# Kernel optimization log

Measured on AMD Instinct MI355X. Metric: run time of the kernel, lower is better.

## Reference

```python
import jax, jax.numpy as jnp
import numpy as np

N_DIM = 32
N_HEADS = 4
HEAD_SIZE = N_DIM // N_HEADS  # 8


def setup_inputs() -> dict:
    key = jax.random.key(0)
    ks = jax.random.split(key, 9)
    B, T = 16, 2048
    s = 1.0 / np.sqrt(N_DIM)
    inp = {
        "x": jax.random.normal(ks[0], (B, T, N_DIM), dtype=jnp.float32),
        "Wq": jax.random.uniform(ks[1], (N_DIM, N_DIM), jnp.float32, -s, s),
        "bq": jax.random.uniform(ks[2], (N_DIM,), jnp.float32, -s, s),
        "Wk": jax.random.uniform(ks[3], (N_DIM, N_DIM), jnp.float32, -s, s),
        "bk": jax.random.uniform(ks[4], (N_DIM,), jnp.float32, -s, s),
        "Wv": jax.random.uniform(ks[5], (N_DIM, N_DIM), jnp.float32, -s, s),
        "bv": jax.random.uniform(ks[6], (N_DIM,), jnp.float32, -s, s),
        "Wp": jax.random.uniform(ks[7], (N_DIM, N_DIM), jnp.float32, -s, s),
        "bp": jax.random.uniform(ks[8], (N_DIM,), jnp.float32, -s, s),
    }
    return inp


def reference(x, Wq, bq, Wk, bk, Wv, bv, Wp, bp):
    b, t, c = x.shape
    # nn.Linear: y = x @ W^T + b
    def heads(W, bias):
        y = jnp.einsum("btc,dc->btd", x, W) + bias
        return y.reshape(b, t, N_HEADS, HEAD_SIZE).transpose(0, 2, 1, 3)  # [b,h,t,d]

    q = heads(Wq, bq)
    k = heads(Wk, bk)
    v = heads(Wv, bv)

    scores = jnp.einsum("bhqd,bhkd->bhqk", q, k) / np.sqrt(HEAD_SIZE)  # [b,h,t,t]
    causal = jnp.tril(jnp.ones((t, t), dtype=bool))
    scores = jnp.where(causal[None, None], scores, -jnp.inf)
    weights = jax.nn.softmax(scores, axis=-1)
    # dropout layers are identity in eval mode
    z = jnp.einsum("bhqk,bhkd->bhqd", weights, v)
    z = z.transpose(0, 2, 1, 3).reshape(b, t, N_DIM)
    z = jnp.einsum("btc,dc->btd", z, Wp) + bp
    return z
```

## Files before the change

### kernel.cpp

```cpp
#include <hip/hip_runtime.h>
#include <math.h>

#define BB 16
#define TT 2048
#define CC 32
#define HH 4
#define DD 8

#define KBS 2056
#define VRS 264
#define VBS (9 * VRS)
#define ZP 33

typedef __fp16 h2  __attribute__((ext_vector_type(2)));
typedef __fp16 h8  __attribute__((ext_vector_type(8)));
typedef float  fx16 __attribute__((ext_vector_type(16)));
typedef int    i4v __attribute__((ext_vector_type(4)));

__device__ __forceinline__ h2 pkh(float a, float b) {
#if __has_builtin(__builtin_amdgcn_cvt_pkrtz)
    return __builtin_amdgcn_cvt_pkrtz(a, b);
#else
    h2 r; r.x = (__fp16)a; r.y = (__fp16)b; return r;
#endif
}

__device__ __forceinline__ float fexp2(float x) {
#if __has_builtin(__builtin_amdgcn_exp2f)
    return __builtin_amdgcn_exp2f(x);
#else
    return exp2f(x);
#endif
}

__device__ __forceinline__ int h2bits(h2 v) { return __builtin_bit_cast(int, v); }

__device__ __forceinline__ void makeP(const fx16& S, bool last, int thr, int hi, h8* P) {
    float pe[16];
    #pragma unroll
    for (int r = 0; r < 16; r++) {
        const int ko = (r & 3) + 8 * (r >> 2);
        float sv = S[r];
        if (last) sv = (ko <= thr) ? sv : -INFINITY;
        pe[r] = fexp2(sv);
    }
    int Hh[8];
    #pragma unroll
    for (int i = 0; i < 8; i++) Hh[i] = h2bits(pkh(pe[2*i], pe[2*i+1]));
    #pragma unroll
    for (int s = 0; s < 2; s++) {
        const int b0 = 4 * s;
        int own0 = hi ? Hh[b0+2] : Hh[b0+0];
        int own1 = hi ? Hh[b0+3] : Hh[b0+1];
        int snd0 = hi ? Hh[b0+0] : Hh[b0+2];
        int snd1 = hi ? Hh[b0+1] : Hh[b0+3];
        int rcv0 = __shfl_xor(snd0, 32);
        int rcv1 = __shfl_xor(snd1, 32);
        i4v f;
        f.x = hi ? rcv0 : own0;
        f.y = hi ? rcv1 : own1;
        f.z = hi ? own0 : rcv0;
        f.w = hi ? own1 : rcv1;
        P[s] = __builtin_bit_cast(h8, f);
    }
}

__global__ __launch_bounds__(256) void qkv_kernel(
    const float* __restrict__ x,
    const float* __restrict__ Wq, const float* __restrict__ bq,
    const float* __restrict__ Wk, const float* __restrict__ bk,
    const float* __restrict__ Wv, const float* __restrict__ bv,
    __fp16* __restrict__ Qo, __fp16* __restrict__ Ko, __fp16* __restrict__ Vo)
{
    __shared__ float Xs[256 * ZP];
    const int tid = threadIdx.x;
    const int m = blockIdx.y >> 2, h = blockIdx.y & 3;
    const int row0 = blockIdx.x * 256;

    {
        const float4* xg = (const float4*)(x + (size_t)row0 * CC);
        #pragma unroll
        for (int i = 0; i < 8; i++) {
            const int idx = tid + 256 * i;
            float4 f = xg[idx];
            const int w = idx * 4;
            float* d = &Xs[(w >> 5) * ZP + (w & 31)];
            d[0] = f.x; d[1] = f.y; d[2] = f.z; d[3] = f.w;
        }
    }
    __syncthreads();

    const int row = row0 + tid;
    const int b = row >> 11, t = row & 2047;
    const int bh = b * HH + h;

    float xr[CC];
    #pragma unroll
    for (int c = 0; c < CC; c++) xr[c] = Xs[tid * ZP + c];

    const float* W    = (m == 0) ? Wq : (m == 1) ? Wk : Wv;
    const float* bias = (m == 0) ? bq : (m == 1) ? bk : bv;

    float o[DD];
    #pragma unroll
    for (int d = 0; d < DD; d++) {
        const int dd = h * DD + d;
        float acc = bias[dd];
        #pragma unroll
        for (int c = 0; c < CC; c++) acc += xr[c] * W[dd * CC + c];
        o[d] = acc;
    }

    if (m == 0) {
        const float qs = 0.3535533905932738f * 1.4426950408889634f;
        i4v qw;
        qw.x = h2bits(pkh(o[0]*qs, o[1]*qs)); qw.y = h2bits(pkh(o[2]*qs, o[3]*qs));
        qw.z = h2bits(pkh(o[4]*qs, o[5]*qs)); qw.w = h2bits(pkh(o[6]*qs, o[7]*qs));
        *(i4v*)(Qo + ((size_t)bh * TT + t) * DD) = qw;
    } else if (m == 1) {
        i4v kw;
        kw.x = h2bits(pkh(o[0], o[1])); kw.y = h2bits(pkh(o[2], o[3]));
        kw.z = h2bits(pkh(o[4], o[5])); kw.w = h2bits(pkh(o[6], o[7]));
        *(i4v*)(Ko + ((size_t)bh * TT + t) * DD) = kw;
    } else {
        __fp16* vt = Vo + (size_t)bh * 9 * TT + t;
        #pragma unroll
        for (int d = 0; d < DD; d++) vt[d * TT] = (__fp16)o[d];
        vt[8 * TT] = (__fp16)1.0f;
    }
}

__global__ __launch_bounds__(256, 2) void attn_kernel(
    const __fp16* __restrict__ Qg, const __fp16* __restrict__ Kg,
    const __fp16* __restrict__ Vg,
    const float* __restrict__ Wp, const float* __restrict__ bp,
    float* __restrict__ out)
{
    __shared__ __align__(16) __fp16 KsS[4 * KBS];
    __shared__ __align__(16) __fp16 VtS[4 * VBS];
    __shared__ float zbuf[64 * ZP];

    const int tid  = threadIdx.x;
    const int b    = blockIdx.x & 15;
    const int ip   = blockIdx.x >> 4;
    const int h    = tid >> 6;
    const int lane = tid & 63;
    const int qc   = lane & 31;
    const int hi   = lane >> 5;

    const int bh  = b * HH + h;
    const int qb1 = 32 * ip;
    const int qb2 = 32 * (63 - ip);
    const int keys_needed = qb2 + 32;
    const int nst = (keys_needed + 255) >> 8;

    h8 qf1, qf2;
    {
        h8 qz;
        #pragma unroll
        for (int i = 0; i < 8; i++) qz[i] = (__fp16)0.0f;
        h8 qa = *(const h8*)(Qg + ((size_t)bh * TT + qb1 + qc) * DD);
        h8 qb = *(const h8*)(Qg + ((size_t)bh * TT + qb2 + qc) * DD);
        qf1 = hi ? qz : qa;
        qf2 = hi ? qz : qb;
    }

    fx16 O1, O2, zc;
    #pragma unroll
    for (int i = 0; i < 16; i++) { O1[i] = 0.0f; O2[i] = 0.0f; zc[i] = 0.0f; }

    const int vrow = (qc < 9) ? qc : 8;
    const int thr  = qc - 4 * hi;

    const __fp16* kgl = Kg + (size_t)bh * TT * DD;
    const __fp16* vgl = Vg + (size_t)bh * 9 * TT;
    __fp16* kld = KsS + h * KBS;
    __fp16* vld = VtS + h * VBS;
    const __fp16* kb = kld + qc * DD;
    const __fp16* vb = vld + vrow * VRS + 8 * hi;

    i4v kpre[4], vpre[5];
    {
        const i4v* ks = (const i4v*)kgl;
        #pragma unroll
        for (int r = 0; r < 4; r++) kpre[r] = ks[lane + 64 * r];
        #pragma unroll
        for (int r = 0; r < 5; r++) {
            int i = lane + 64 * r; if (i > 287) i = 287;
            vpre[r] = *(const i4v*)(vgl + (i >> 5) * TT + (i & 31) * 8);
        }
    }

    for (int sti = 0; sti < nst; sti++) {
        const int st = sti * 256;
        {
            i4v* kd = (i4v*)kld;
            #pragma unroll
            for (int r = 0; r < 4; r++) kd[lane + 64 * r] = kpre[r];
            #pragma unroll
            for (int r = 0; r < 5; r++) {
                const int i = lane + 64 * r;
                if (i < 288) *(i4v*)(vld + (i >> 5) * VRS + (i & 31) * 8) = vpre[r];
            }
        }
        if (sti + 1 < nst) {
            const int st2 = st + 256;
            const i4v* ks = (const i4v*)(kgl + (size_t)st2 * DD);
            #pragma unroll
            for (int r = 0; r < 4; r++) kpre[r] = ks[lane + 64 * r];
            #pragma unroll
            for (int r = 0; r < 5; r++) {
                int i = lane + 64 * r; if (i > 287) i = 287;
                vpre[r] = *(const i4v*)(vgl + (i >> 5) * TT + st2 + (i & 31) * 8);
            }
        }

        const int kend = min(st + 256, keys_needed);
        for (int kt = st; kt < kend; kt += 32) {
            const bool a1 = (kt <= qb1);
            h8 kf = *(const h8*)(kb + (kt - st) * DD);

            h8 P1[2], P2[2];
            if (a1) {
                fx16 S = __builtin_amdgcn_mfma_f32_32x32x16_f16(kf, qf1, zc, 0, 0, 0);
                makeP(S, kt == qb1, thr, hi, P1);
            }
            {
                fx16 S = __builtin_amdgcn_mfma_f32_32x32x16_f16(kf, qf2, zc, 0, 0, 0);
                makeP(S, kt == qb2, thr, hi, P2);
            }
            #pragma unroll
            for (int s = 0; s < 2; s++) {
                h8 vf = *(const h8*)(vb + (kt - st) + 16 * s);
                if (a1) O1 = __builtin_amdgcn_mfma_f32_32x32x16_f16(vf, P1[s], O1, 0, 0, 0);
                O2 = __builtin_amdgcn_mfma_f32_32x32x16_f16(vf, P2[s], O2, 0, 0, 0);
            }
        }
    }

    {
        const float i1 = 1.0f / O1[4], i2 = 1.0f / O2[4];
        float* z1 = &zbuf[qc * ZP + h * DD + 4 * hi];
        float* z2 = &zbuf[(32 + qc) * ZP + h * DD + 4 * hi];
        z1[0] = O1[0]*i1; z1[1] = O1[1]*i1; z1[2] = O1[2]*i1; z1[3] = O1[3]*i1;
        z2[0] = O2[0]*i2; z2[1] = O2[1]*i2; z2[2] = O2[2]*i2; z2[3] = O2[3]*i2;
    }
    __syncthreads();

    {
        const int seg = tid >> 6;
        const int r = tid & 63;
        float zr[CC];
        #pragma unroll
        for (int c = 0; c < CC; c++) zr[c] = zbuf[r * ZP + c];
        float o[DD];
        #pragma unroll
        for (int d = 0; d < DD; d++) {
            const int dd = seg * DD + d;
            float acc = bp[dd];
            #pragma unroll
            for (int c = 0; c < CC; c++) acc += zr[c] * Wp[dd * CC + c];
            o[d] = acc;
        }
        const int qglob = (r < 32) ? (ip * 32 + r) : ((63 - ip) * 32 + (r - 32));
        float* dst = out + ((size_t)b * TT + qglob) * CC + seg * DD;
        ((float4*)dst)[0] = make_float4(o[0], o[1], o[2], o[3]);
        ((float4*)dst)[1] = make_float4(o[4], o[5], o[6], o[7]);
    }
}

extern "C" void kernel_launch(void* const* d_in, const int* in_sizes, int n_in,
                              void* d_out, int out_size, void* d_ws, size_t ws_size,
                              hipStream_t stream) {
    const float* x  = (const float*)d_in[0];
    const float* Wq = (const float*)d_in[1];
    const float* bq = (const float*)d_in[2];
    const float* Wk = (const float*)d_in[3];
    const float* bk = (const float*)d_in[4];
    const float* Wv = (const float*)d_in[5];
    const float* bv = (const float*)d_in[6];
    const float* Wp = (const float*)d_in[7];
    const float* bp = (const float*)d_in[8];
    float* out = (float*)d_out;

    const size_t NE = (size_t)BB * HH * TT * DD;
    __fp16* Qh = (__fp16*)d_ws;
    __fp16* Kh = Qh + NE;
    __fp16* Vt = Kh + NE;

    qkv_kernel<<<dim3(BB * TT / 256, 12), 256, 0, stream>>>(x, Wq, bq, Wk, bk, Wv, bv, Qh, Kh, Vt);
    attn_kernel<<<dim3(BB * 32), 256, 0, stream>>>(Qh, Kh, Vt, Wp, bp, out);
}
```

Before: 111.9 us.

## Split paired query tiles across separate waves with 512-thread attention blocks

Each attention block now runs 8 waves instead of 4. Each wave handles one head and one of the two paired query tiles (early or late), where before one wave handled both tiles in sequence. This raises wave-level parallelism and shortens the per-wave critical path. In exchange, K/V tiles are staged into LDS twice (once per wave pair), LDS use doubles, and waves within a block become imbalanced because the early-tile wave finishes sooner. The output projection is split across 8 segments of 4 columns each.

Result: slower. 127.3 us (+13.7%).

```diff
diff --git a/kernel.cpp b/kernel.cpp
--- a/kernel.cpp
+++ b/kernel.cpp
@@ -130,52 +130,51 @@
     }
 }
 
-__global__ __launch_bounds__(256, 2) void attn_kernel(
+__global__ __launch_bounds__(512, 4) void attn_kernel(
     const __fp16* __restrict__ Qg, const __fp16* __restrict__ Kg,
     const __fp16* __restrict__ Vg,
     const float* __restrict__ Wp, const float* __restrict__ bp,
     float* __restrict__ out)
 {
-    __shared__ __align__(16) __fp16 KsS[4 * KBS];
-    __shared__ __align__(16) __fp16 VtS[4 * VBS];
+    __shared__ __align__(16) __fp16 KsS[8 * KBS];
+    __shared__ __align__(16) __fp16 VtS[8 * VBS];
     __shared__ float zbuf[64 * ZP];
 
     const int tid  = threadIdx.x;
     const int b    = blockIdx.x & 15;
     const int ip   = blockIdx.x >> 4;
-    const int h    = tid >> 6;
+    const int w    = tid >> 6;
+    const int h    = w & 3;
+    const int qsel = w >> 2;
     const int lane = tid & 63;
     const int qc   = lane & 31;
     const int hi   = lane >> 5;
 
     const int bh  = b * HH + h;
-    const int qb1 = 32 * ip;
-    const int qb2 = 32 * (63 - ip);
-    const int keys_needed = qb2 + 32;
+    const int qb  = 32 * (qsel ? (63 - ip) : ip);
+    const int keys_needed = qb + 32;
     const int nst = (keys_needed + 255) >> 8;
 
-    h8 qf1, qf2;
+    h8 qf;
     {
         h8 qz;
         #pragma unroll
         for (int i = 0; i < 8; i++) qz[i] = (__fp16)0.0f;
-        h8 qa = *(const h8*)(Qg + ((size_t)bh * TT + qb1 + qc) * DD);
-        h8 qb = *(const h8*)(Qg + ((size_t)bh * TT + qb2 + qc) * DD);
-        qf1 = hi ? qz : qa;
-        qf2 = hi ? qz : qb;
-    }
-
-    fx16 O1, O2, zc;
-    #pragma unroll
-    for (int i = 0; i < 16; i++) { O1[i] = 0.0f; O2[i] = 0.0f; zc[i] = 0.0f; }
+        h8 qa = *(const h8*)(Qg + ((size_t)bh * TT + qb + qc) * DD);
+        qf = hi ? qz : qa;
+    }
+
+    fx16 O, zc;
+    #pragma unroll
+    for (int i = 0; i < 16; i++) { O[i] = 0.0f; zc[i] = 0.0f; }
 
     const int vrow = (qc < 9) ? qc : 8;
     const int thr  = qc - 4 * hi;
 
     const __fp16* kgl = Kg + (size_t)bh * TT * DD;
     const __fp16* vgl = Vg + (size_t)bh * 9 * TT;
-    __fp16* kld = KsS + h * KBS;
-    __fp16* vld = VtS + h * VBS;
+    __fp16* kld = KsS + w * KBS;
+    __fp16* vld = VtS + w * VBS;
     const __fp16* kb = kld + qc * DD;
     const __fp16* vb = vld + vrow * VRS + 8 * hi;
 
@@ -217,33 +216,22 @@
 
         const int kend = min(st + 256, keys_needed);
         for (int kt = st; kt < kend; kt += 32) {
-            const bool a1 = (kt <= qb1);
             h8 kf = *(const h8*)(kb + (kt - st) * DD);
-
-            h8 P1[2], P2[2];
-            if (a1) {
-                fx16 S = __builtin_amdgcn_mfma_f32_32x32x16_f16(kf, qf1, zc, 0, 0, 0);
-                makeP(S, kt == qb1, thr, hi, P1);
-            }
-            {
-                fx16 S = __builtin_amdgcn_mfma_f32_32x32x16_f16(kf, qf2, zc, 0, 0, 0);
-                makeP(S, kt == qb2, thr, hi, P2);
-            }
+            fx16 S = __builtin_amdgcn_mfma_f32_32x32x16_f16(kf, qf, zc, 0, 0, 0);
+            h8 P[2];
+            makeP(S, kt == qb, thr, hi, P);
             #pragma unroll
             for (int s = 0; s < 2; s++) {
                 h8 vf = *(const h8*)(vb + (kt - st) + 16 * s);
-                if (a1) O1 = __builtin_amdgcn_mfma_f32_32x32x16_f16(vf, P1[s], O1, 0, 0, 0);
-                O2 = __builtin_amdgcn_mfma_f32_32x32x16_f16(vf, P2[s], O2, 0, 0, 0);
+                O = __builtin_amdgcn_mfma_f32_32x32x16_f16(vf, P[s], O, 0, 0, 0);
             }
         }
     }
 
     {
-        const float i1 = 1.0f / O1[4], i2 = 1.0f / O2[4];
-        float* z1 = &zbuf[qc * ZP + h * DD + 4 * hi];
-        float* z2 = &zbuf[(32 + qc) * ZP + h * DD + 4 * hi];
-        z1[0] = O1[0]*i1; z1[1] = O1[1]*i1; z1[2] = O1[2]*i1; z1[3] = O1[3]*i1;
-        z2[0] = O2[0]*i2; z2[1] = O2[1]*i2; z2[2] = O2[2]*i2; z2[3] = O2[3]*i2;
+        const float inv = 1.0f / O[4];
+        float* z = &zbuf[(qsel * 32 + qc) * ZP + h * DD + 4 * hi];
+        z[0] = O[0]*inv; z[1] = O[1]*inv; z[2] = O[2]*inv; z[3] = O[3]*inv;
     }
     __syncthreads();
 
@@ -253,19 +241,18 @@
         float zr[CC];
         #pragma unroll
         for (int c = 0; c < CC; c++) zr[c] = zbuf[r * ZP + c];
-        float o[DD];
-        #pragma unroll
-        for (int d = 0; d < DD; d++) {
-            const int dd = seg * DD + d;
+        float o[4];
+        #pragma unroll
+        for (int d = 0; d < 4; d++) {
+            const int dd = seg * 4 + d;
             float acc = bp[dd];
             #pragma unroll
             for (int c = 0; c < CC; c++) acc += zr[c] * Wp[dd * CC + c];
             o[d] = acc;
         }
         const int qglob = (r < 32) ? (ip * 32 + r) : ((63 - ip) * 32 + (r - 32));
-        float* dst = out + ((size_t)b * TT + qglob) * CC + seg * DD;
-        ((float4*)dst)[0] = make_float4(o[0], o[1], o[2], o[3]);
-        ((float4*)dst)[1] = make_float4(o[4], o[5], o[6], o[7]);
+        float* dst = out + ((size_t)b * TT + qglob) * CC + seg * 4;
+        *(float4*)dst = make_float4(o[0], o[1], o[2], o[3]);
     }
 }
 
@@ -289,5 +276,5 @@
     __fp16* Vt = Kh + NE;
 
     qkv_kernel<<<dim3(BB * TT / 256, 12), 256, 0, stream>>>(x, Wq, bq, Wk, bk, Wv, bv, Qh, Kh, Vt);
-    attn_kernel<<<dim3(BB * 32), 256, 0, stream>>>(Qh, Kh, Vt, Wp, bp, out);
-}
+    attn_kernel<<<dim3(BB * 32), 512, 0, stream>>>(Qh, Kh, Vt, Wp, bp, out);
+}
```

## Compute QKV projection with fp16 MFMA and use permlane32 swap in softmax

Applied to the files above, without the earlier changes.

The QKV projection kernel is rewritten so each wave computes a 32-row by 32-output tile with two 32x32x16 fp16 MFMAs, replacing the scalar FMA loops over shared-memory-staged x. Each block of three waves handles Q, K and V for 32 rows, with fragments rearranged across half-waves before packed stores. The attention kernel's P-fragment construction uses permlane32_swap instead of two shuffles plus selects when the builtin is available. Inputs and weights are now rounded to fp16 before the projection, which lowers precision, and the V path writes with scattered 2-byte stores.

Result: faster. 106.0 us (-5.3%).

```diff
diff --git a/kernel.cpp b/kernel.cpp
--- a/kernel.cpp
+++ b/kernel.cpp
@@ -16,6 +16,7 @@
 typedef __fp16 h8  __attribute__((ext_vector_type(8)));
 typedef float  fx16 __attribute__((ext_vector_type(16)));
 typedef int    i4v __attribute__((ext_vector_type(4)));
+typedef int    i2v __attribute__((ext_vector_type(2)));
 
 __device__ __forceinline__ h2 pkh(float a, float b) {
 #if __has_builtin(__builtin_amdgcn_cvt_pkrtz)
@@ -35,6 +36,13 @@
 
 __device__ __forceinline__ int h2bits(h2 v) { return __builtin_bit_cast(int, v); }
 
+__device__ __forceinline__ h8 pk8(float4 a, float4 b) {
+    i4v f;
+    f.x = h2bits(pkh(a.x, a.y)); f.y = h2bits(pkh(a.z, a.w));
+    f.z = h2bits(pkh(b.x, b.y)); f.w = h2bits(pkh(b.z, b.w));
+    return __builtin_bit_cast(h8, f);
+}
+
 __device__ __forceinline__ void makeP(const fx16& S, bool last, int thr, int hi, h8* P) {
     float pe[16];
     #pragma unroll
@@ -47,6 +55,19 @@
     int Hh[8];
     #pragma unroll
     for (int i = 0; i < 8; i++) Hh[i] = h2bits(pkh(pe[2*i], pe[2*i+1]));
+#if __has_builtin(__builtin_amdgcn_permlane32_swap)
+    #pragma unroll
+    for (int s = 0; s < 2; s++) {
+        const int b0 = 4 * s;
+        auto ra = __builtin_amdgcn_permlane32_swap(Hh[b0+0], Hh[b0+2], false, false);
+        auto rb = __builtin_amdgcn_permlane32_swap(Hh[b0+1], Hh[b0+3], false, false);
+        i2v pa = __builtin_bit_cast(i2v, ra);
+        i2v pb = __builtin_bit_cast(i2v, rb);
+        i4v f;
+        f.x = pa.x; f.y = pb.x; f.z = pa.y; f.w = pb.y;
+        P[s] = __builtin_bit_cast(h8, f);
+    }
+#else
     #pragma unroll
     for (int s = 0; s < 2; s++) {
         const int b0 = 4 * s;
@@ -63,70 +84,109 @@
         f.w = hi ? own1 : rcv1;
         P[s] = __builtin_bit_cast(h8, f);
     }
-}
-
-__global__ __launch_bounds__(256) void qkv_kernel(
+#endif
+}
+
+__global__ __launch_bounds__(192, 3) void qkv_kernel(
     const float* __restrict__ x,
     const float* __restrict__ Wq, const float* __restrict__ bq,
     const float* __restrict__ Wk, const float* __restrict__ bk,
     const float* __restrict__ Wv, const float* __restrict__ bv,
     __fp16* __restrict__ Qo, __fp16* __restrict__ Ko, __fp16* __restrict__ Vo)
 {
-    __shared__ float Xs[256 * ZP];
-    const int tid = threadIdx.x;
-    const int m = blockIdx.y >> 2, h = blockIdx.y & 3;
-    const int row0 = blockIdx.x * 256;
-
-    {
-        const float4* xg = (const float4*)(x + (size_t)row0 * CC);
-        #pragma unroll
-        for (int i = 0; i < 8; i++) {
-            const int idx = tid + 256 * i;
-            float4 f = xg[idx];
-            const int w = idx * 4;
-            float* d = &Xs[(w >> 5) * ZP + (w & 31)];
-            d[0] = f.x; d[1] = f.y; d[2] = f.z; d[3] = f.w;
-        }
-    }
-    __syncthreads();
-
-    const int row = row0 + tid;
-    const int b = row >> 11, t = row & 2047;
-    const int bh = b * HH + h;
-
-    float xr[CC];
-    #pragma unroll
-    for (int c = 0; c < CC; c++) xr[c] = Xs[tid * ZP + c];
+    const int tid  = threadIdx.x;
+    const int m    = tid >> 6;
+    const int lane = tid & 63;
+    const int qc   = lane & 31;
+    const int hi   = lane >> 5;
+
+    const int row = blockIdx.x * 32 + qc;
+    const int b   = row >> 11, t = row & 2047;
 
     const float* W    = (m == 0) ? Wq : (m == 1) ? Wk : Wv;
     const float* bias = (m == 0) ? bq : (m == 1) ? bk : bv;
 
-    float o[DD];
-    #pragma unroll
-    for (int d = 0; d < DD; d++) {
-        const int dd = h * DD + d;
-        float acc = bias[dd];
-        #pragma unroll
-        for (int c = 0; c < CC; c++) acc += xr[c] * W[dd * CC + c];
-        o[d] = acc;
-    }
-
+    const float* xr = x + (size_t)row * CC + 8 * hi;
+    h8 B0 = pk8(*(const float4*)(xr),      *(const float4*)(xr + 4));
+    h8 B1 = pk8(*(const float4*)(xr + 16), *(const float4*)(xr + 20));
+
+    const float* wr = W + (size_t)qc * CC + 8 * hi;
+    h8 A0 = pk8(*(const float4*)(wr),      *(const float4*)(wr + 4));
+    h8 A1 = pk8(*(const float4*)(wr + 16), *(const float4*)(wr + 20));
+
+    fx16 zc;
+    #pragma unroll
+    for (int i = 0; i < 16; i++) zc[i] = 0.0f;
+    fx16 D = __builtin_amdgcn_mfma_f32_32x32x16_f16(A0, B0, zc, 0, 0, 0);
+    D = __builtin_amdgcn_mfma_f32_32x32x16_f16(A1, B1, D, 0, 0, 0);
+
+    float o[16];
+    {
+        float4 bb0 = *(const float4*)(bias + 0  + 4 * hi);
+        float4 bb1 = *(const float4*)(bias + 8  + 4 * hi);
+        float4 bb2 = *(const float4*)(bias + 16 + 4 * hi);
+        float4 bb3 = *(const float4*)(bias + 24 + 4 * hi);
+        const float* bbp[1];
+        o[0] = D[0] + bb0.x; o[1] = D[1] + bb0.y; o[2]  = D[2]  + bb0.z; o[3]  = D[3]  + bb0.w;
+        o[4] = D[4] + bb1.x; o[5] = D[5] + bb1.y; o[6]  = D[6]  + bb1.z; o[7]  = D[7]  + bb1.w;
+        o[8] = D[8] + bb2.x; o[9] = D[9] + bb2.y; o[10] = D[10] + bb2.z; o[11] = D[11] + bb2.w;
+        o[12] = D[12] + bb3.x; o[13] = D[13] + bb3.y; o[14] = D[14] + bb3.z; o[15] = D[15] + bb3.w;
+        (void)bbp;
+    }
     if (m == 0) {
         const float qs = 0.3535533905932738f * 1.4426950408889634f;
-        i4v qw;
-        qw.x = h2bits(pkh(o[0]*qs, o[1]*qs)); qw.y = h2bits(pkh(o[2]*qs, o[3]*qs));
-        qw.z = h2bits(pkh(o[4]*qs, o[5]*qs)); qw.w = h2bits(pkh(o[6]*qs, o[7]*qs));
-        *(i4v*)(Qo + ((size_t)bh * TT + t) * DD) = qw;
-    } else if (m == 1) {
-        i4v kw;
-        kw.x = h2bits(pkh(o[0], o[1])); kw.y = h2bits(pkh(o[2], o[3]));
-        kw.z = h2bits(pkh(o[4], o[5])); kw.w = h2bits(pkh(o[6], o[7]));
-        *(i4v*)(Ko + ((size_t)bh * TT + t) * DD) = kw;
+        #pragma unroll
+        for (int r = 0; r < 16; r++) o[r] *= qs;
+    }
+
+    if (m == 2) {
+        #pragma unroll
+        for (int r = 0; r < 16; r++) {
+            const int h = r >> 2, d = (r & 3) + 4 * hi;
+            Vo[(((size_t)(b * HH + h)) * 9 + d) * TT + t] = (__fp16)o[r];
+        }
+        const int hA = hi ? 2 : 0, hB = hi ? 3 : 1;
+        Vo[(((size_t)(b * HH + hA)) * 9 + 8) * TT + t] = (__fp16)1.0f;
+        Vo[(((size_t)(b * HH + hB)) * 9 + 8) * TT + t] = (__fp16)1.0f;
     } else {
-        __fp16* vt = Vo + (size_t)bh * 9 * TT + t;
-        #pragma unroll
-        for (int d = 0; d < DD; d++) vt[d * TT] = (__fp16)o[d];
-        vt[8 * TT] = (__fp16)1.0f;
+        int I0[4], I1[4];
+        #pragma unroll
+        for (int g = 0; g < 4; g++) {
+            I0[g] = h2bits(pkh(o[4*g + 0], o[4*g + 1]));
+            I1[g] = h2bits(pkh(o[4*g + 2], o[4*g + 3]));
+        }
+        i4v fr0, fr1, fr2, fr3;
+#if __has_builtin(__builtin_amdgcn_permlane32_swap)
+    #define MAKE_FRAG(g, out) { \
+        auto ra = __builtin_amdgcn_permlane32_swap(I0[g], I1[g], false, false); \
+        auto rb = __builtin_amdgcn_permlane32_swap(I1[g], I0[g], false, false); \
+        i2v p1 = __builtin_bit_cast(i2v, ra); \
+        i2v p2 = __builtin_bit_cast(i2v, rb); \
+        i4v f; \
+        f.x = hi ? p2.x : p1.x;   \
+        f.y = hi ? p1.x : p2.x;   \
+        f.z = hi ? p2.y : p1.y;   \
+        f.w = hi ? p1.y : p2.y;   \
+        out = f; }
+#else
+    #define MAKE_FRAG(g, out) { \
+        int s0 = __shfl_xor(I0[g], 32); \
+        int s1 = __shfl_xor(I1[g], 32); \
+        i4v f; \
+        f.x = hi ? s0 : I0[g]; \
+        f.y = hi ? s1 : I1[g]; \
+        f.z = hi ? I0[g] : s0; \
+        f.w = hi ? I1[g] : s1; \
+        out = f; }
+#endif
+        MAKE_FRAG(0, fr0); MAKE_FRAG(1, fr1); MAKE_FRAG(2, fr2); MAKE_FRAG(3, fr3);
+    #undef MAKE_FRAG
+        i4v fA = hi ? fr2 : fr0;
+        i4v fB = hi ? fr3 : fr1;
+        const int gA = hi ? 2 : 0, gB = hi ? 3 : 1;
+        __fp16* O = (m == 0) ? Qo : Ko;
+        *(i4v*)(O + ((size_t)(b * HH + gA) * TT + t) * DD) = fA;
+        *(i4v*)(O + ((size_t)(b * HH + gB) * TT + t) * DD) = fB;
     }
 }
 
@@ -288,6 +348,6 @@
     __fp16* Kh = Qh + NE;
     __fp16* Vt = Kh + NE;
 
-    qkv_kernel<<<dim3(BB * TT / 256, 12), 256, 0, stream>>>(x, Wq, bq, Wk, bk, Wv, bv, Qh, Kh, Vt);
+    qkv_kernel<<<dim3(BB * TT / 32), 192, 0, stream>>>(x, Wq, bq, Wk, bk, Wv, bv, Qh, Kh, Vt);
     attn_kernel<<<dim3(BB * 32), 256, 0, stream>>>(Qh, Kh, Vt, Wp, bp, out);
 }
```

## Fuse QKV projection into attention kernel, recomputing K/V per key tile via MFMA

Applied to the files above, without the earlier changes.

Removes the separate QKV kernel and its fp16 workspace round trip. Each attention block now projects Q, K and V on the fly from x using MFMA with fp16-packed weights. V is written into a small double-buffered LDS slot per key tile, and the next tile of x is prefetched. The cross-half-wave exchange uses permlane32_swap where the builtin is available. In exchange, every block redundantly recomputes K and V for all keys it needs, and LDS writes and reads of V happen within a wave without an explicit barrier.

Result: slower. 130.3 us (+16.5%).

```diff
diff --git a/kernel.cpp b/kernel.cpp
--- a/kernel.cpp
+++ b/kernel.cpp
@@ -7,15 +7,15 @@
 #define HH 4
 #define DD 8
 
-#define KBS 2056
-#define VRS 264
-#define VBS (9 * VRS)
+#define VR2 88
+#define VBS2 (9 * VR2)
 #define ZP 33
 
 typedef __fp16 h2  __attribute__((ext_vector_type(2)));
 typedef __fp16 h8  __attribute__((ext_vector_type(8)));
 typedef float  fx16 __attribute__((ext_vector_type(16)));
 typedef int    i4v __attribute__((ext_vector_type(4)));
+typedef int    i2v __attribute__((ext_vector_type(2)));
 
 __device__ __forceinline__ h2 pkh(float a, float b) {
 #if __has_builtin(__builtin_amdgcn_cvt_pkrtz)
@@ -34,6 +34,31 @@
 }
 
 __device__ __forceinline__ int h2bits(h2 v) { return __builtin_bit_cast(int, v); }
+
+__device__ __forceinline__ h8 pk8(float4 a, float4 b) {
+    i4v f;
+    f.x = h2bits(pkh(a.x, a.y)); f.y = h2bits(pkh(a.z, a.w));
+    f.z = h2bits(pkh(b.x, b.y)); f.w = h2bits(pkh(b.z, b.w));
+    return __builtin_bit_cast(h8, f);
+}
+
+__device__ __forceinline__ h8 rowfrag(float o0, float o1, float o2, float o3, int hi) {
+    int I0 = h2bits(pkh(o0, o1));
+    int I1 = h2bits(pkh(o2, o3));
+    i4v f;
+#if __has_builtin(__builtin_amdgcn_permlane32_swap)
+    auto ra = __builtin_amdgcn_permlane32_swap(I0, I0, false, false);
+    auto rb = __builtin_amdgcn_permlane32_swap(I1, I1, false, false);
+    i2v pa = __builtin_bit_cast(i2v, ra);
+    i2v pb = __builtin_bit_cast(i2v, rb);
+    f.x = I0; f.y = I1; f.z = pa.y; f.w = pb.y;
+#else
+    int s0 = __shfl_xor(I0, 32), s1 = __shfl_xor(I1, 32);
+    f.x = hi ? s0 : I0; f.y = hi ? s1 : I1;
+    f.z = hi ? I0 : s0; f.w = hi ? I1 : s1;
+#endif
+    return __builtin_bit_cast(h8, f);
+}
 
 __device__ __forceinline__ void makeP(const fx16& S, bool last, int thr, int hi, h8* P) {
     float pe[16];
@@ -47,6 +72,19 @@
     int Hh[8];
     #pragma unroll
     for (int i = 0; i < 8; i++) Hh[i] = h2bits(pkh(pe[2*i], pe[2*i+1]));
+#if __has_builtin(__builtin_amdgcn_permlane32_swap)
+    #pragma unroll
+    for (int s = 0; s < 2; s++) {
+        const int b0 = 4 * s;
+        auto ra = __builtin_amdgcn_permlane32_swap(Hh[b0+0], Hh[b0+2], false, false);
+        auto rb = __builtin_amdgcn_permlane32_swap(Hh[b0+1], Hh[b0+3], false, false);
+        i2v pa = __builtin_bit_cast(i2v, ra);
+        i2v pb = __builtin_bit_cast(i2v, rb);
+        i4v f;
+        f.x = pa.x; f.y = pb.x; f.z = pa.y; f.w = pb.y;
+        P[s] = __builtin_bit_cast(h8, f);
+    }
+#else
     #pragma unroll
     for (int s = 0; s < 2; s++) {
         const int b0 = 4 * s;
@@ -63,81 +101,28 @@
         f.w = hi ? own1 : rcv1;
         P[s] = __builtin_bit_cast(h8, f);
     }
-}
-
-__global__ __launch_bounds__(256) void qkv_kernel(
+#endif
+}
+
+struct XP { float4 a, b, c, d; };
+__device__ __forceinline__ XP load_xpack(const float* __restrict__ x,
+                                         int bTT, int t, int hi) {
+    const float* xr = x + (size_t)(bTT + t) * CC + 8 * hi;
+    XP p;
+    p.a = *(const float4*)(xr);      p.b = *(const float4*)(xr + 4);
+    p.c = *(const float4*)(xr + 16); p.d = *(const float4*)(xr + 20);
+    return p;
+}
+
+__global__ __launch_bounds__(256, 2) void attn_kernel(
     const float* __restrict__ x,
     const float* __restrict__ Wq, const float* __restrict__ bq,
     const float* __restrict__ Wk, const float* __restrict__ bk,
     const float* __restrict__ Wv, const float* __restrict__ bv,
-    __fp16* __restrict__ Qo, __fp16* __restrict__ Ko, __fp16* __restrict__ Vo)
-{
-    __shared__ float Xs[256 * ZP];
-    const int tid = threadIdx.x;
-    const int m = blockIdx.y >> 2, h = blockIdx.y & 3;
-    const int row0 = blockIdx.x * 256;
-
-    {
-        const float4* xg = (const float4*)(x + (size_t)row0 * CC);
-        #pragma unroll
-        for (int i = 0; i < 8; i++) {
-            const int idx = tid + 256 * i;
-            float4 f = xg[idx];
-            const int w = idx * 4;
-            float* d = &Xs[(w >> 5) * ZP + (w & 31)];
-            d[0] = f.x; d[1] = f.y; d[2] = f.z; d[3] = f.w;
-        }
-    }
-    __syncthreads();
-
-    const int row = row0 + tid;
-    const int b = row >> 11, t = row & 2047;
-    const int bh = b * HH + h;
-
-    float xr[CC];
-    #pragma unroll
-    for (int c = 0; c < CC; c++) xr[c] = Xs[tid * ZP + c];
-
-    const float* W    = (m == 0) ? Wq : (m == 1) ? Wk : Wv;
-    const float* bias = (m == 0) ? bq : (m == 1) ? bk : bv;
-
-    float o[DD];
-    #pragma unroll
-    for (int d = 0; d < DD; d++) {
-        const int dd = h * DD + d;
-        float acc = bias[dd];
-        #pragma unroll
-        for (int c = 0; c < CC; c++) acc += xr[c] * W[dd * CC + c];
-        o[d] = acc;
-    }
-
-    if (m == 0) {
-        const float qs = 0.3535533905932738f * 1.4426950408889634f;
-        i4v qw;
-        qw.x = h2bits(pkh(o[0]*qs, o[1]*qs)); qw.y = h2bits(pkh(o[2]*qs, o[3]*qs));
-        qw.z = h2bits(pkh(o[4]*qs, o[5]*qs)); qw.w = h2bits(pkh(o[6]*qs, o[7]*qs));
-        *(i4v*)(Qo + ((size_t)bh * TT + t) * DD) = qw;
-    } else if (m == 1) {
-        i4v kw;
-        kw.x = h2bits(pkh(o[0], o[1])); kw.y = h2bits(pkh(o[2], o[3]));
-        kw.z = h2bits(pkh(o[4], o[5])); kw.w = h2bits(pkh(o[6], o[7]));
-        *(i4v*)(Ko + ((size_t)bh * TT + t) * DD) = kw;
-    } else {
-        __fp16* vt = Vo + (size_t)bh * 9 * TT + t;
-        #pragma unroll
-        for (int d = 0; d < DD; d++) vt[d * TT] = (__fp16)o[d];
-        vt[8 * TT] = (__fp16)1.0f;
-    }
-}
-
-__global__ __launch_bounds__(256, 2) void attn_kernel(
-    const __fp16* __restrict__ Qg, const __fp16* __restrict__ Kg,
-    const __fp16* __restrict__ Vg,
     const float* __restrict__ Wp, const float* __restrict__ bp,
     float* __restrict__ out)
 {
-    __shared__ __align__(16) __fp16 KsS[4 * KBS];
-    __shared__ __align__(16) __fp16 VtS[4 * VBS];
+    __shared__ __align__(16) __fp16 VtS[4 * VBS2];
     __shared__ float zbuf[64 * ZP];
 
     const int tid  = threadIdx.x;
@@ -148,93 +133,115 @@
     const int qc   = lane & 31;
     const int hi   = lane >> 5;
 
-    const int bh  = b * HH + h;
+    const int bTT = b * TT;
     const int qb1 = 32 * ip;
     const int qb2 = 32 * (63 - ip);
     const int keys_needed = qb2 + 32;
-    const int nst = (keys_needed + 255) >> 8;
+
+    const int wrow = 8 * h + (qc & 7);
+    h8 KA0, KA1, VA0, VA1, QA0, QA1;
+    {
+        const float* wr = Wk + (size_t)wrow * CC + 8 * hi;
+        KA0 = pk8(*(const float4*)(wr),      *(const float4*)(wr + 4));
+        KA1 = pk8(*(const float4*)(wr + 16), *(const float4*)(wr + 20));
+        wr = Wv + (size_t)wrow * CC + 8 * hi;
+        VA0 = pk8(*(const float4*)(wr),      *(const float4*)(wr + 4));
+        VA1 = pk8(*(const float4*)(wr + 16), *(const float4*)(wr + 20));
+        wr = Wq + (size_t)wrow * CC + 8 * hi;
+        QA0 = pk8(*(const float4*)(wr),      *(const float4*)(wr + 4));
+        QA1 = pk8(*(const float4*)(wr + 16), *(const float4*)(wr + 20));
+    }
+    const float4 bk4 = *(const float4*)(bk + 8 * h + 4 * hi);
+    const float4 bv4 = *(const float4*)(bv + 8 * h + 4 * hi);
+    const float4 bq4 = *(const float4*)(bq + 8 * h + 4 * hi);
+
+    fx16 zc;
+    #pragma unroll
+    for (int i = 0; i < 16; i++) zc[i] = 0.0f;
 
     h8 qf1, qf2;
     {
         h8 qz;
         #pragma unroll
         for (int i = 0; i < 8; i++) qz[i] = (__fp16)0.0f;
-        h8 qa = *(const h8*)(Qg + ((size_t)bh * TT + qb1 + qc) * DD);
-        h8 qb = *(const h8*)(Qg + ((size_t)bh * TT + qb2 + qc) * DD);
-        qf1 = hi ? qz : qa;
-        qf2 = hi ? qz : qb;
-    }
-
-    fx16 O1, O2, zc;
-    #pragma unroll
-    for (int i = 0; i < 16; i++) { O1[i] = 0.0f; O2[i] = 0.0f; zc[i] = 0.0f; }
+        const float qs = 0.3535533905932738f * 1.4426950408889634f;
+        {
+            XP xp = load_xpack(x, bTT, qb1 + qc, hi);
+            h8 B0 = pk8(xp.a, xp.b), B1 = pk8(xp.c, xp.d);
+            fx16 D = __builtin_amdgcn_mfma_f32_32x32x16_f16(QA0, B0, zc, 0, 0, 0);
+            D = __builtin_amdgcn_mfma_f32_32x32x16_f16(QA1, B1, D, 0, 0, 0);
+            h8 f = rowfrag((D[0]+bq4.x)*qs, (D[1]+bq4.y)*qs,
+                           (D[2]+bq4.z)*qs, (D[3]+bq4.w)*qs, hi);
+            qf1 = hi ? qz : f;
+        }
+        {
+            XP xp = load_xpack(x, bTT, qb2 + qc, hi);
+            h8 B0 = pk8(xp.a, xp.b), B1 = pk8(xp.c, xp.d);
+            fx16 D = __builtin_amdgcn_mfma_f32_32x32x16_f16(QA0, B0, zc, 0, 0, 0);
+            D = __builtin_amdgcn_mfma_f32_32x32x16_f16(QA1, B1, D, 0, 0, 0);
+            h8 f = rowfrag((D[0]+bq4.x)*qs, (D[1]+bq4.y)*qs,
+                           (D[2]+bq4.z)*qs, (D[3]+bq4.w)*qs, hi);
+            qf2 = hi ? qz : f;
+        }
+    }
+
+    fx16 O1, O2;
+    #pragma unroll
+    for (int i = 0; i < 16; i++) { O1[i] = 0.0f; O2[i] = 0.0f; }
 
     const int vrow = (qc < 9) ? qc : 8;
     const int thr  = qc - 4 * hi;
 
-    const __fp16* kgl = Kg + (size_t)bh * TT * DD;
-    const __fp16* vgl = Vg + (size_t)bh * 9 * TT;
-    __fp16* kld = KsS + h * KBS;
-    __fp16* vld = VtS + h * VBS;
-    const __fp16* kb = kld + qc * DD;
-    const __fp16* vb = vld + vrow * VRS + 8 * hi;
-
-    i4v kpre[4], vpre[5];
-    {
-        const i4v* ks = (const i4v*)kgl;
-        #pragma unroll
-        for (int r = 0; r < 4; r++) kpre[r] = ks[lane + 64 * r];
-        #pragma unroll
-        for (int r = 0; r < 5; r++) {
-            int i = lane + 64 * r; if (i > 287) i = 287;
-            vpre[r] = *(const i4v*)(vgl + (i >> 5) * TT + (i & 31) * 8);
-        }
-    }
-
-    for (int sti = 0; sti < nst; sti++) {
-        const int st = sti * 256;
-        {
-            i4v* kd = (i4v*)kld;
-            #pragma unroll
-            for (int r = 0; r < 4; r++) kd[lane + 64 * r] = kpre[r];
-            #pragma unroll
-            for (int r = 0; r < 5; r++) {
-                const int i = lane + 64 * r;
-                if (i < 288) *(i4v*)(vld + (i >> 5) * VRS + (i & 31) * 8) = vpre[r];
-            }
-        }
-        if (sti + 1 < nst) {
-            const int st2 = st + 256;
-            const i4v* ks = (const i4v*)(kgl + (size_t)st2 * DD);
-            #pragma unroll
-            for (int r = 0; r < 4; r++) kpre[r] = ks[lane + 64 * r];
-            #pragma unroll
-            for (int r = 0; r < 5; r++) {
-                int i = lane + 64 * r; if (i > 287) i = 287;
-                vpre[r] = *(const i4v*)(vgl + (i >> 5) * TT + st2 + (i & 31) * 8);
-            }
-        }
-
-        const int kend = min(st + 256, keys_needed);
-        for (int kt = st; kt < kend; kt += 32) {
-            const bool a1 = (kt <= qb1);
-            h8 kf = *(const h8*)(kb + (kt - st) * DD);
-
-            h8 P1[2], P2[2];
-            if (a1) {
-                fx16 S = __builtin_amdgcn_mfma_f32_32x32x16_f16(kf, qf1, zc, 0, 0, 0);
-                makeP(S, kt == qb1, thr, hi, P1);
-            }
-            {
-                fx16 S = __builtin_amdgcn_mfma_f32_32x32x16_f16(kf, qf2, zc, 0, 0, 0);
-                makeP(S, kt == qb2, thr, hi, P2);
-            }
-            #pragma unroll
-            for (int s = 0; s < 2; s++) {
-                h8 vf = *(const h8*)(vb + (kt - st) + 16 * s);
-                if (a1) O1 = __builtin_amdgcn_mfma_f32_32x32x16_f16(vf, P1[s], O1, 0, 0, 0);
-                O2 = __builtin_amdgcn_mfma_f32_32x32x16_f16(vf, P2[s], O2, 0, 0, 0);
-            }
+    __fp16* vld = VtS + h * VBS2;
+    const __fp16* vbase = vld + vrow * VR2 + 8 * hi;
+
+    {
+        if (lane < 40) *(h2*)(vld + 8 * VR2 + lane * 2) = h2{(__fp16)1.0f, (__fp16)1.0f};
+    }
+
+    XP xnext = load_xpack(x, bTT, 0 + qc, hi);
+
+    for (int kt = 0; kt < keys_needed; kt += 32) {
+        const int slot = (kt >> 5) & 1;
+        const XP xc = xnext;
+        {
+            const int ktn = (kt + 32 < keys_needed) ? kt + 32 : 0;
+            xnext = load_xpack(x, bTT, ktn + qc, hi);
+        }
+        h8 B0 = pk8(xc.a, xc.b), B1 = pk8(xc.c, xc.d);
+
+        h8 kf;
+        {
+            fx16 Dk = __builtin_amdgcn_mfma_f32_32x32x16_f16(KA0, B0, zc, 0, 0, 0);
+            Dk = __builtin_amdgcn_mfma_f32_32x32x16_f16(KA1, B1, Dk, 0, 0, 0);
+            kf = rowfrag(Dk[0]+bk4.x, Dk[1]+bk4.y, Dk[2]+bk4.z, Dk[3]+bk4.w, hi);
+        }
+
+        {
+            fx16 Dv = __builtin_amdgcn_mfma_f32_32x32x16_f16(VA0, B0, zc, 0, 0, 0);
+            Dv = __builtin_amdgcn_mfma_f32_32x32x16_f16(VA1, B1, Dv, 0, 0, 0);
+            __fp16* vw = vld + (size_t)(4 * hi) * VR2 + slot * 40 + qc;
+            vw[0 * VR2] = (__fp16)(Dv[0] + bv4.x);
+            vw[1 * VR2] = (__fp16)(Dv[1] + bv4.y);
+            vw[2 * VR2] = (__fp16)(Dv[2] + bv4.z);
+            vw[3 * VR2] = (__fp16)(Dv[3] + bv4.w);
+        }
+
+        const bool a1 = (kt <= qb1);
+        h8 P1[2], P2[2];
+        if (a1) {
+            fx16 S = __builtin_amdgcn_mfma_f32_32x32x16_f16(kf, qf1, zc, 0, 0, 0);
+            makeP(S, kt == qb1, thr, hi, P1);
+        }
+        {
+            fx16 S = __builtin_amdgcn_mfma_f32_32x32x16_f16(kf, qf2, zc, 0, 0, 0);
+            makeP(S, kt == qb2, thr, hi, P2);
+        }
+        #pragma unroll
+        for (int s = 0; s < 2; s++) {
+            h8 vf = *(const h8*)(vbase + slot * 40 + 16 * s);
+            if (a1) O1 = __builtin_amdgcn_mfma_f32_32x32x16_f16(vf, P1[s], O1, 0, 0, 0);
+            O2 = __builtin_amdgcn_mfma_f32_32x32x16_f16(vf, P2[s], O2, 0, 0, 0);
         }
     }
 
@@ -282,12 +289,8 @@
     const float* Wp = (const float*)d_in[7];
     const float* bp = (const float*)d_in[8];
     float* out = (float*)d_out;
-
-    const size_t NE = (size_t)BB * HH * TT * DD;
-    __fp16* Qh = (__fp16*)d_ws;
-    __fp16* Kh = Qh + NE;
-    __fp16* Vt = Kh + NE;
-
-    qkv_kernel<<<dim3(BB * TT / 256, 12), 256, 0, stream>>>(x, Wq, bq, Wk, bk, Wv, bv, Qh, Kh, Vt);
-    attn_kernel<<<dim3(BB * 32), 256, 0, stream>>>(Qh, Kh, Vt, Wp, bp, out);
-}
+    (void)d_ws; (void)ws_size; (void)in_sizes; (void)n_in; (void)out_size;
+
+    attn_kernel<<<dim3(BB * 32), 256, 0, stream>>>(
+        x, Wq, bq, Wk, bk, Wv, bv, Wp, bp, out);
+}
```
